# Optimization experiments

Hardware: AMD Instinct MI355X
Metric: run time of the kernel (lower is better)

## Reference

```python
import jax, jax.numpy as jnp
import numpy as np

K_SCHEDULE = (4, 8, 16)


def setup_inputs() -> dict:
    key = jax.random.key(0)
    B, T, D = 2, 2048, 1024
    R = len(K_SCHEDULE)
    kx, = jax.random.split(key, 1)
    return {
        "x": jax.random.normal(kx, (B, T, D), dtype=jnp.float32),
        "gain": jnp.ones((R, D), dtype=jnp.float32),
        "bias": jnp.zeros((R, D), dtype=jnp.float32),
        "log_mix": jnp.zeros((R,), dtype=jnp.float32),
        "log_momentum": jnp.asarray(1.0, dtype=jnp.float32),
        "log_scale": jnp.asarray(0.0, dtype=jnp.float32),
    }


def _round(h, K, gain_r, bias_r, mix, momentum):
    B, T, D = h.shape
    # causal top-K adjacency from evolving hidden state
    scores = jnp.einsum("bid,bjd->bij", h, h)                      # (B,T,T)
    causal = jnp.tril(jnp.ones((T, T), dtype=bool))                # j <= i
    masked = jnp.where(causal[None], scores, -jnp.inf)
    vals, idx = jax.lax.top_k(masked, K)                           # (B,T,K)
    valid = jnp.isfinite(vals)                                     # early rows have < K causal neighbors
    # unweighted (mean) neighbor aggregation via gather
    gathered = jnp.take_along_axis(h[:, None, :, :], idx[..., None], axis=2)  # (B,T,K,D)
    vf = valid.astype(h.dtype)
    count = jnp.maximum(vf.sum(-1, keepdims=True), 1.0)            # (B,T,1)
    msg = (gathered * vf[..., None]).sum(axis=2) / count           # (B,T,D)
    # gated residual blend + affine + GELU + momentum update
    blended = mix * h + (1.0 - mix) * msg
    h_new = jax.nn.gelu(blended * gain_r + bias_r, approximate=False)
    return momentum * h + (1.0 - momentum) * h_new


def reference(x, gain, bias, log_mix, log_momentum, log_scale):
    momentum = jax.nn.sigmoid(log_momentum)
    scale = jax.nn.softplus(log_scale) + 0.01
    h = x
    for r, K_r in enumerate(K_SCHEDULE):
        mix = jax.nn.sigmoid(log_mix[r])
        h = _round(h, K_r, gain[r], bias[r], mix, momentum)
    return (h - x) * scale
```

## Files before the change

kernel.cpp:

```cpp
#include <hip/hip_runtime.h>
#include <math.h>

#define BB 2
#define TT 2048
#define DD 1024
#define NTHREADS 256

#define RT 64
#define CT 128
#define DC 32
#define NCHUNK (DD / DC)
#define NJC (TT / CT)
#define KMAX 16
#define CST 132
#define NTILES 272
#define NROWS (BB * TT)
#define CSLAB ((uint32_t)(NROWS * DC))
#define PLANE ((uint32_t)(BB * TT * DD))
#define B0 0
#define B1 12288
#define B2 24576


typedef _Float16 half8  __attribute__((ext_vector_type(8)));
typedef _Float16 half4v __attribute__((ext_vector_type(4)));
typedef float    float4v __attribute__((ext_vector_type(4)));

#define GLD16(gp, lp) __builtin_amdgcn_global_load_lds(                         \
    (const __attribute__((address_space(1))) unsigned int*)(gp),                \
    (__attribute__((address_space(3))) unsigned int*)(lp), 16, 0, 0)

__device__ __forceinline__ float gelu_exact(float t) {
    return 0.5f * t * (1.0f + erff(t * 0.70710678118654752f));
}

__global__ __launch_bounds__(NTHREADS) void split_kernel(
    const float* __restrict__ h,
    _Float16* __restrict__ hiP,
    _Float16* __restrict__ loP)
{
    const int idx = blockIdx.x * NTHREADS + threadIdx.x;
    const float4 v = ((const float4*)h)[idx];
    const float xs[4] = {v.x, v.y, v.z, v.w};
    half4v hi, lo;
    #pragma unroll
    for (int u = 0; u < 4; ++u) {
        const _Float16 hh = (_Float16)xs[u];
        hi[u] = hh;
        lo[u] = (_Float16)(xs[u] - (float)hh);
    }
    const uint32_t tot  = (uint32_t)idx * 4u;
    const uint32_t grow = tot >> 10;
    const uint32_t wh   = tot & 1023u;
    const uint32_t off  = ((wh >> 5) * (uint32_t)NROWS + grow) * 32u + (wh & 31u);
    *(half4v*)(hiP + off) = hi;
    *(half4v*)(loP + off) = lo;
}

__global__ __launch_bounds__(NTHREADS) void score_topk_kernel(
    const _Float16* __restrict__ hiP,
    float* __restrict__ pval,
    int*   __restrict__ pidx,
    int K)
{
    __shared__ __align__(16) char smem_raw[73728];
    _Float16* sm  = (_Float16*)smem_raw;
    float* scores = (float*)smem_raw;

    const int b = blockIdx.y;
    const int p = blockIdx.x;
    int g = (int)(0.5f * (sqrtf(4.0f * (float)p + 1.0f) - 1.0f));
    while ((g + 1) * (g + 2) <= p) ++g;
    while (g * (g + 1) > p) --g;
    const int qq = p - g * (g + 1);
    const int it = 2 * g + qq / (g + 1);
    const int jc = qq % (g + 1);
    const int i0 = it * RT, j0 = jc * CT;

    const int tid  = threadIdx.x;
    const int lane = tid & 63, wave = tid >> 6;
    const int wr = wave & 1, wc = wave >> 1;

    uint32_t goff[6];
    #pragma unroll
    for (int slot = 0; slot < 6; ++slot) {
        const int gr = tid + NTHREADS * slot;
        int n, row; uint32_t pl;
        if (gr < 256)       { n = gr;        pl = 0; row = i0 + 16 * (n >> 6) + (n & 15); }
        else if (gr < 512)  { n = gr - 256;  pl = 1; row = i0 + 16 * (n >> 6) + (n & 15); }
        else if (gr < 1024) { n = gr - 512;  pl = 0; row = j0 + 16 * (n >> 6) + (n & 15); }
        else                { n = gr - 1024; pl = 1; row = j0 + 16 * (n >> 6) + (n & 15); }
        const int oct = (n >> 4) & 3;
        goff[slot] = pl * PLANE + (uint32_t)(b * TT + row) * DC + (uint32_t)oct * 8;
    }

    float4v acc[2][4];
    #pragma unroll
    for (int rb = 0; rb < 2; ++rb)
        #pragma unroll
        for (int cb = 0; cb < 4; ++cb)
            acc[rb][cb] = (float4v){0.f, 0.f, 0.f, 0.f};

    #pragma unroll
    for (int t = 0; t < 6; ++t)
        GLD16(hiP + goff[t], &sm[B0 + (size_t)(tid + NTHREADS * t) * 8]);
    #pragma unroll
    for (int t = 0; t < 6; ++t)
        GLD16(hiP + goff[t] + CSLAB, &sm[B1 + (size_t)(tid + NTHREADS * t) * 8]);

#define CHUNK1B(c, BCUR, BNXT, VMSTR, DO_ISSUE) do {                              \
        asm volatile("s_waitcnt vmcnt(" VMSTR ")" ::: "memory");                  \
        __builtin_amdgcn_s_barrier();                                             \
        asm volatile("" ::: "memory");                                            \
        if (DO_ISSUE) {                                                           \
            _Pragma("unroll")                                                     \
            for (int t = 0; t < 6; ++t)                                           \
                GLD16(hiP + goff[t] + (uint32_t)((c) + 2) * CSLAB,                \
                      &sm[(BNXT) + (size_t)(tid + NTHREADS * t) * 8]);            \
        }                                                                         \
        __builtin_amdgcn_sched_barrier(0);                                        \
        half8 ah[2], al[2], bh[4], bl[4];                                         \
        _Pragma("unroll")                                                         \
        for (int rb = 0; rb < 2; ++rb) {                                          \
            const int band = 2 * wr + rb;                                         \
            ah[rb] = *(const half8*)&sm[(BCUR) +        (band * 64 + lane) * 8];  \
            al[rb] = *(const half8*)&sm[(BCUR) + 2048 + (band * 64 + lane) * 8];  \
        }                                                                         \
        _Pragma("unroll")                                                         \
        for (int cb = 0; cb < 4; ++cb) {                                          \
            const int band = 4 * wc + cb;                                         \
            bh[cb] = *(const half8*)&sm[(BCUR) + 4096 + (band * 64 + lane) * 8];  \
            bl[cb] = *(const half8*)&sm[(BCUR) + 8192 + (band * 64 + lane) * 8];  \
        }                                                                         \
        asm volatile("s_waitcnt lgkmcnt(0)" ::: "memory");                        \
        __builtin_amdgcn_sched_barrier(0);                                        \
        __builtin_amdgcn_s_setprio(1);                                            \
        _Pragma("unroll")                                                         \
        for (int rb = 0; rb < 2; ++rb)                                            \
            _Pragma("unroll")                                                     \
            for (int cb = 0; cb < 4; ++cb) {                                      \
                acc[rb][cb] = __builtin_amdgcn_mfma_f32_16x16x32_f16(             \
                    ah[rb], bh[cb], acc[rb][cb], 0, 0, 0);                        \
                acc[rb][cb] = __builtin_amdgcn_mfma_f32_16x16x32_f16(             \
                    ah[rb], bl[cb], acc[rb][cb], 0, 0, 0);                        \
                acc[rb][cb] = __builtin_amdgcn_mfma_f32_16x16x32_f16(             \
                    al[rb], bh[cb], acc[rb][cb], 0, 0, 0);                        \
            }                                                                     \
        __builtin_amdgcn_s_setprio(0);                                            \
    } while (0)

    for (int ct = 0; ct < 10; ++ct) {
        CHUNK1B(3 * ct + 0, B0, B2, "6", 1);
        CHUNK1B(3 * ct + 1, B1, B0, "6", 1);
        CHUNK1B(3 * ct + 2, B2, B1, "6", 1);
    }
    CHUNK1B(30, B0, B2, "6", 0);
    CHUNK1B(31, B1, B0, "0", 0);
#undef CHUNK1B

    __syncthreads();

    {
        const int qn = lane >> 4, rn = lane & 15;
        #pragma unroll
        for (int rb = 0; rb < 2; ++rb)
            #pragma unroll
            for (int cb = 0; cb < 4; ++cb)
                #pragma unroll
                for (int reg = 0; reg < 4; ++reg) {
                    const int i_loc = 32 * wr + 16 * rb + qn * 4 + reg;
                    const int j_loc = 64 * wc + 16 * cb + rn;
                    scores[i_loc * CST + j_loc] =
                        (j0 + j_loc <= i0 + i_loc) ? acc[rb][cb][reg] : -INFINITY;
                }
    }
    __syncthreads();

    const int rloc = tid >> 2, seg = tid & 3;
    const float* Crow = scores + rloc * CST;
    float vals[32];
    #pragma unroll
    for (int cc = 0; cc < 32; ++cc) vals[cc] = Crow[seg + 4 * cc];

    uint32_t dead = 0;
    const int irow = i0 + rloc;
    const size_t obase = ((size_t)(b * TT + irow) * NJC + jc) * KMAX;
    for (int k = 0; k < K; ++k) {
        float bv = -INFINITY; int bcc = -1;
        #pragma unroll
        for (int cc = 0; cc < 32; ++cc) {
            const bool alive = ((dead >> cc) & 1u) == 0u;
            if (alive && vals[cc] > bv) { bv = vals[cc]; bcc = cc; }
        }
        const int bcol = (bcc >= 0) ? (seg + 4 * bcc) : -1;
        float wv = bv; int wcol = bcol;
        #pragma unroll
        for (int m = 1; m < 4; m <<= 1) {
            const float ov = __shfl_xor(wv, m, 64);
            const int   oc = __shfl_xor(wcol, m, 64);
            if (ov > wv || (ov == wv && (unsigned)oc < (unsigned)wcol)) { wv = ov; wcol = oc; }
        }
        if (seg == 0) {
            pval[obase + k] = wv;
            pidx[obase + k] = (wcol >= 0) ? (j0 + wcol) : -1;
        }
        if (bcc >= 0 && wcol == bcol) dead |= (1u << bcc);
    }
}

template<int K>
__global__ __launch_bounds__(NTHREADS) void merge_agg_kernel(
    const float* __restrict__ h_in,
    float* __restrict__ h_out,
    const float* __restrict__ pval,
    const int*   __restrict__ pidx,
    const float* __restrict__ gain,
    const float* __restrict__ bias,
    const float* __restrict__ log_mix_r,
    const float* __restrict__ log_momentum,
    const float* __restrict__ xres,
    const float* __restrict__ log_scale,
    _Float16* __restrict__ hiO,
    _Float16* __restrict__ loO)
{
    constexpr int KL = (K == 4) ? 2 : (K == 8) ? 3 : 4;
    __shared__ __align__(16) float s_cval[NTHREADS];
    __shared__ __align__(16) int   s_cidx[NTHREADS];
    __shared__ int s_sel[KMAX];

    const int row = blockIdx.x, b = row / TT, i = row % TT;
    const int tid = threadIdx.x;
    const float* hb = h_in + (size_t)b * TT * DD;

    const int count = (i + 1 < K) ? (i + 1) : K;
    const int jcn = i / CT + 1;
    const int ncand = jcn * K;

    float mv = -INFINITY; int mj = -1;
    if (tid < ncand) {
        const int w = tid >> KL, k = tid & (K - 1);
        const size_t base = ((size_t)(b * TT + i) * NJC + w) * KMAX + k;
        const int j = pidx[base];
        if (j >= 0) { mj = j; mv = pval[base]; }
    }
    s_cval[tid] = mv;
    s_cidx[tid] = mj;

    const float4 hi = ((const float4*)(hb + (size_t)i * DD))[tid];
    const float4 g4 = ((const float4*)gain)[tid];
    const float4 c4 = ((const float4*)bias)[tid];
    __syncthreads();

    if (mj >= 0) {
        const int nb = (ncand + 3) >> 2;
        int rank = 0;
        for (int q = 0; q < nb; ++q) {
            const float4 v4 = ((const float4*)s_cval)[q];
            const int4  j4 = ((const int4*)s_cidx)[q];
            rank += (v4.x > mv || (v4.x == mv && (unsigned)j4.x < (unsigned)mj));
            rank += (v4.y > mv || (v4.y == mv && (unsigned)j4.y < (unsigned)mj));
            rank += (v4.z > mv || (v4.z == mv && (unsigned)j4.z < (unsigned)mj));
            rank += (v4.w > mv || (v4.w == mv && (unsigned)j4.w < (unsigned)mj));
        }
        if (rank < count) s_sel[rank] = mj;
    }
    __syncthreads();

    const float mix      = 1.0f / (1.0f + expf(-log_mix_r[0]));
    const float momentum = 1.0f / (1.0f + expf(-log_momentum[0]));
    const float inv_cnt  = 1.0f / (float)count;

    float4 msg = make_float4(0.f, 0.f, 0.f, 0.f);
    if (count == K) {
        #pragma unroll
        for (int k = 0; k < K; ++k) {
            const float4 v = ((const float4*)(hb + (size_t)s_sel[k] * DD))[tid];
            msg.x += v.x; msg.y += v.y; msg.z += v.z; msg.w += v.w;
        }
    } else {
        for (int k = 0; k < count; ++k) {
            const float4 v = ((const float4*)(hb + (size_t)s_sel[k] * DD))[tid];
            msg.x += v.x; msg.y += v.y; msg.z += v.z; msg.w += v.w;
        }
    }

    float4 o;
    {
        float m, t;
        m = msg.x * inv_cnt; t = (mix * hi.x + (1.f - mix) * m) * g4.x + c4.x;
        o.x = momentum * hi.x + (1.f - momentum) * gelu_exact(t);
        m = msg.y * inv_cnt; t = (mix * hi.y + (1.f - mix) * m) * g4.y + c4.y;
        o.y = momentum * hi.y + (1.f - momentum) * gelu_exact(t);
        m = msg.z * inv_cnt; t = (mix * hi.z + (1.f - mix) * m) * g4.z + c4.z;
        o.z = momentum * hi.z + (1.f - momentum) * gelu_exact(t);
        m = msg.w * inv_cnt; t = (mix * hi.w + (1.f - mix) * m) * g4.w + c4.w;
        o.w = momentum * hi.w + (1.f - momentum) * gelu_exact(t);
    }

    if (hiO != nullptr) {
        const float os[4] = {o.x, o.y, o.z, o.w};
        half4v hv, lv;
        #pragma unroll
        for (int u = 0; u < 4; ++u) {
            const _Float16 hh = (_Float16)os[u];
            hv[u] = hh;
            lv[u] = (_Float16)(os[u] - (float)hh);
        }
        const uint32_t wh  = (uint32_t)tid * 4u;
        const uint32_t off = ((wh >> 5) * (uint32_t)NROWS + (uint32_t)row) * 32u + (wh & 31u);
        *(half4v*)(hiO + off) = hv;
        *(half4v*)(loO + off) = lv;
    }

    if (xres != nullptr) {
        const float scale = log1pf(expf(log_scale[0])) + 0.01f;
        const float4 xv = ((const float4*)(xres + (size_t)row * DD))[tid];
        o.x = (o.x - xv.x) * scale;
        o.y = (o.y - xv.y) * scale;
        o.z = (o.z - xv.z) * scale;
        o.w = (o.w - xv.w) * scale;
    }
    ((float4*)(h_out + (size_t)row * DD))[tid] = o;
}

extern "C" void kernel_launch(void* const* d_in, const int* in_sizes, int n_in,
                              void* d_out, int out_size, void* d_ws, size_t ws_size,
                              hipStream_t stream) {
    const float* x            = (const float*)d_in[0];
    const float* gain         = (const float*)d_in[1];
    const float* bias         = (const float*)d_in[2];
    const float* log_mix      = (const float*)d_in[3];
    const float* log_momentum = (const float*)d_in[4];
    const float* log_scale    = (const float*)d_in[5];
    float* out = (float*)d_out;

    char* wsb = (char*)d_ws;
    float*     h_ws = (float*)wsb;
    float*     pval = (float*)(wsb + (size_t)BB * TT * DD * 4);
    int*       pidx = (int*)  (wsb + (size_t)BB * TT * DD * 4 + (size_t)BB * TT * NJC * KMAX * 4);
    _Float16*  hiP  = (_Float16*)(wsb + (size_t)BB * TT * DD * 4 + (size_t)BB * TT * NJC * KMAX * 8);
    _Float16*  loP  = hiP + (size_t)PLANE;

    const dim3 sgrid(NTILES, BB);
    const int nsplit = BB * TT * DD / 4 / NTHREADS;

    split_kernel<<<nsplit, NTHREADS, 0, stream>>>(x, hiP, loP);
    score_topk_kernel<<<sgrid, NTHREADS, 0, stream>>>(hiP, pval, pidx, 4);
    merge_agg_kernel<4><<<BB * TT, NTHREADS, 0, stream>>>(
        x, out, pval, pidx, gain + 0 * DD, bias + 0 * DD, log_mix + 0, log_momentum,
        nullptr, nullptr, hiP, loP);
    score_topk_kernel<<<sgrid, NTHREADS, 0, stream>>>(hiP, pval, pidx, 8);
    merge_agg_kernel<8><<<BB * TT, NTHREADS, 0, stream>>>(
        out, h_ws, pval, pidx, gain + 1 * DD, bias + 1 * DD, log_mix + 1, log_momentum,
        nullptr, nullptr, hiP, loP);
    score_topk_kernel<<<sgrid, NTHREADS, 0, stream>>>(hiP, pval, pidx, 16);
    merge_agg_kernel<16><<<BB * TT, NTHREADS, 0, stream>>>(
        h_ws, out, pval, pidx, gain + 2 * DD, bias + 2 * DD, log_mix + 2, log_momentum,
        x, log_scale, nullptr, nullptr);
}
```

Measured before the change: 311.2 us.

## Load A operands directly to registers and double-buffer only B tiles in LDS

The A-side (row) fragments are now fetched straight from global memory into registers with inline global_load_dwordx4, using two register sets for even and odd chunks. Only the B-side column tiles still go through LDS, so the triple buffer becomes a double buffer and shared memory drops from 72KB to 33KB. This should allow more resident blocks per CU and cut LDS traffic. The cost is an extra barrier per chunk before the next B tile overwrites the current buffer, plus more vector registers and a hand-tuned vmcnt accounting that mixes LDS-direct and register loads.

```diff
diff --git a/kernel.cpp b/kernel.cpp
--- a/kernel.cpp
+++ b/kernel.cpp
@@ -17,9 +17,7 @@
 #define NROWS (BB * TT)
 #define CSLAB ((uint32_t)(NROWS * DC))
 #define PLANE ((uint32_t)(BB * TT * DD))
-#define B0 0
-#define B1 12288
-#define B2 24576
+#define HBUF_B 8192
 
 
 typedef _Float16 half8  __attribute__((ext_vector_type(8)));
@@ -29,6 +27,10 @@
 #define GLD16(gp, lp) __builtin_amdgcn_global_load_lds(                         \
     (const __attribute__((address_space(1))) unsigned int*)(gp),                \
     (__attribute__((address_space(3))) unsigned int*)(lp), 16, 0, 0)
+
+#define GLDS(dst, voff, sbase) asm volatile(                                    \
+    "global_load_dwordx4 %0, %1, %2"                                           \
+    : "=v"(dst) : "v"(voff), "s"(sbase) : "memory")
 
 __device__ __forceinline__ float gelu_exact(float t) {
     return 0.5f * t * (1.0f + erff(t * 0.70710678118654752f));
@@ -63,7 +65,7 @@
     int*   __restrict__ pidx,
     int K)
 {
-    __shared__ __align__(16) char smem_raw[73728];
+    __shared__ __align__(16) char smem_raw[33792];
     _Float16* sm  = (_Float16*)smem_raw;
     float* scores = (float*)smem_raw;
 
@@ -81,18 +83,26 @@
     const int lane = tid & 63, wave = tid >> 6;
     const int wr = wave & 1, wc = wave >> 1;
 
-    uint32_t goff[6];
-    #pragma unroll
-    for (int slot = 0; slot < 6; ++slot) {
-        const int gr = tid + NTHREADS * slot;
-        int n, row; uint32_t pl;
-        if (gr < 256)       { n = gr;        pl = 0; row = i0 + 16 * (n >> 6) + (n & 15); }
-        else if (gr < 512)  { n = gr - 256;  pl = 1; row = i0 + 16 * (n >> 6) + (n & 15); }
-        else if (gr < 1024) { n = gr - 512;  pl = 0; row = j0 + 16 * (n >> 6) + (n & 15); }
-        else                { n = gr - 1024; pl = 1; row = j0 + 16 * (n >> 6) + (n & 15); }
+    const _Float16* baseHi = hiP;
+    const _Float16* baseLo = hiP + PLANE;
+
+    uint32_t goffB[4];
+    #pragma unroll
+    for (int s = 0; s < 4; ++s) {
+        const int gr = tid + NTHREADS * s;
+        const uint32_t pl = (uint32_t)(gr >> 9);
+        const int n = gr & 511;
+        const int row = j0 + 16 * (n >> 6) + (n & 15);
         const int oct = (n >> 4) & 3;
-        goff[slot] = pl * PLANE + (uint32_t)(b * TT + row) * DC + (uint32_t)oct * 8;
-    }
+        goffB[s] = pl * PLANE + (uint32_t)(b * TT + row) * DC + (uint32_t)oct * 8;
+    }
+
+    const uint32_t lrow = (uint32_t)(lane & 15);
+    const uint32_t loct = (uint32_t)((lane >> 4) & 3);
+    uint32_t vA[2];
+    #pragma unroll
+    for (int rb = 0; rb < 2; ++rb)
+        vA[rb] = 2u * ((uint32_t)(b * TT + i0 + 16 * (2 * wr + rb) + lrow) * DC + loct * 8u);
 
     float4v acc[2][4];
     #pragma unroll
@@ -101,38 +111,44 @@
         for (int cb = 0; cb < 4; ++cb)
             acc[rb][cb] = (float4v){0.f, 0.f, 0.f, 0.f};
 
-    #pragma unroll
-    for (int t = 0; t < 6; ++t)
-        GLD16(hiP + goff[t], &sm[B0 + (size_t)(tid + NTHREADS * t) * 8]);
-    #pragma unroll
-    for (int t = 0; t < 6; ++t)
-        GLD16(hiP + goff[t] + CSLAB, &sm[B1 + (size_t)(tid + NTHREADS * t) * 8]);
-
-#define CHUNK1B(c, BCUR, BNXT, VMSTR, DO_ISSUE) do {                              \
+    half8 aEh[2], aEl[2];
+    half8 aOh[2], aOl[2];
+
+#define ISSUE_A(AH, AL) do {                                                    \
+        GLDS(AH[0], vA[0], baseHi); GLDS(AL[0], vA[0], baseLo);                 \
+        GLDS(AH[1], vA[1], baseHi); GLDS(AL[1], vA[1], baseLo);                 \
+        vA[0] += 2u * CSLAB; vA[1] += 2u * CSLAB;                               \
+    } while (0)
+
+    #pragma unroll
+    for (int s = 0; s < 4; ++s)
+        GLD16(hiP + goffB[s], &sm[(size_t)(tid + NTHREADS * s) * 8]);
+    ISSUE_A(aEh, aEl);
+    #pragma unroll
+    for (int s = 0; s < 4; ++s)
+        GLD16(hiP + goffB[s] + CSLAB, &sm[HBUF_B + (size_t)(tid + NTHREADS * s) * 8]);
+    ISSUE_A(aOh, aOl);
+
+#define CHUNK_H(c, CUR, AH, AL, VMSTR) do {                                       \
         asm volatile("s_waitcnt vmcnt(" VMSTR ")" ::: "memory");                  \
-        __builtin_amdgcn_s_barrier();                                             \
+        __builtin_amdgcn_s_barrier();              \
         asm volatile("" ::: "memory");                                            \
-        if (DO_ISSUE) {                                                           \
-            _Pragma("unroll")                                                     \
-            for (int t = 0; t < 6; ++t)                                           \
-                GLD16(hiP + goff[t] + (uint32_t)((c) + 2) * CSLAB,                \
-                      &sm[(BNXT) + (size_t)(tid + NTHREADS * t) * 8]);            \
-        }                                                                         \
-        __builtin_amdgcn_sched_barrier(0);                                        \
-        half8 ah[2], al[2], bh[4], bl[4];                                         \
-        _Pragma("unroll")                                                         \
-        for (int rb = 0; rb < 2; ++rb) {                                          \
-            const int band = 2 * wr + rb;                                         \
-            ah[rb] = *(const half8*)&sm[(BCUR) +        (band * 64 + lane) * 8];  \
-            al[rb] = *(const half8*)&sm[(BCUR) + 2048 + (band * 64 + lane) * 8];  \
-        }                                                                         \
+        half8 bh[4], bl[4];                                                       \
         _Pragma("unroll")                                                         \
         for (int cb = 0; cb < 4; ++cb) {                                          \
             const int band = 4 * wc + cb;                                         \
-            bh[cb] = *(const half8*)&sm[(BCUR) + 4096 + (band * 64 + lane) * 8];  \
-            bl[cb] = *(const half8*)&sm[(BCUR) + 8192 + (band * 64 + lane) * 8];  \
+            bh[cb] = *(const half8*)&sm[(CUR) +        (band * 64 + lane) * 8];   \
+            bl[cb] = *(const half8*)&sm[(CUR) + 4096 + (band * 64 + lane) * 8];   \
         }                                                                         \
         asm volatile("s_waitcnt lgkmcnt(0)" ::: "memory");                        \
+        __builtin_amdgcn_s_barrier();                \
+        asm volatile("" ::: "memory");                                            \
+        if ((c) + 2 < NCHUNK) {                   \
+            _Pragma("unroll")                                                     \
+            for (int s = 0; s < 4; ++s)                                           \
+                GLD16(hiP + goffB[s] + (uint32_t)((c) + 2) * CSLAB,               \
+                      &sm[(CUR) + (size_t)(tid + NTHREADS * s) * 8]);             \
+        }                                                                         \
         __builtin_amdgcn_sched_barrier(0);                                        \
         __builtin_amdgcn_s_setprio(1);                                            \
         _Pragma("unroll")                                                         \
@@ -140,23 +156,25 @@
             _Pragma("unroll")                                                     \
             for (int cb = 0; cb < 4; ++cb) {                                      \
                 acc[rb][cb] = __builtin_amdgcn_mfma_f32_16x16x32_f16(             \
-                    ah[rb], bh[cb], acc[rb][cb], 0, 0, 0);                        \
+                    AH[rb], bh[cb], acc[rb][cb], 0, 0, 0);                        \
                 acc[rb][cb] = __builtin_amdgcn_mfma_f32_16x16x32_f16(             \
-                    ah[rb], bl[cb], acc[rb][cb], 0, 0, 0);                        \
+                    AH[rb], bl[cb], acc[rb][cb], 0, 0, 0);                        \
                 acc[rb][cb] = __builtin_amdgcn_mfma_f32_16x16x32_f16(             \
-                    al[rb], bh[cb], acc[rb][cb], 0, 0, 0);                        \
+                    AL[rb], bh[cb], acc[rb][cb], 0, 0, 0);                        \
             }                                                                     \
         __builtin_amdgcn_s_setprio(0);                                            \
+        __builtin_amdgcn_sched_barrier(0);      \
+        if ((c) + 2 < NCHUNK) { ISSUE_A(AH, AL); }                                \
     } while (0)
 
-    for (int ct = 0; ct < 10; ++ct) {
-        CHUNK1B(3 * ct + 0, B0, B2, "6", 1);
-        CHUNK1B(3 * ct + 1, B1, B0, "6", 1);
-        CHUNK1B(3 * ct + 2, B2, B1, "6", 1);
-    }
-    CHUNK1B(30, B0, B2, "6", 0);
-    CHUNK1B(31, B1, B0, "0", 0);
-#undef CHUNK1B
+    for (int cc = 0; cc < 15; ++cc) {
+        CHUNK_H(2 * cc,     0,      aEh, aEl, "8");
+        CHUNK_H(2 * cc + 1, HBUF_B, aOh, aOl, "8");
+    }
+    CHUNK_H(30, 0,      aEh, aEl, "8");
+    CHUNK_H(31, HBUF_B, aOh, aOl, "0");
+#undef CHUNK_H
+#undef ISSUE_A
 
     __syncthreads();
 
```

Result: slower. 319.7 us (+2.7%).
